# Performance work log

Measured on AMD Instinct MI355X. Metric: run time of the kernel, lower is better.

## Reference

```python
import jax, jax.numpy as jnp
import numpy as np

HEADS = 8
WS = 16
EPS = 1e-6


def setup_inputs() -> dict:
    key = jax.random.key(0)
    k1, k2 = jax.random.split(key)
    x = jax.random.normal(k1, (4, 64, 512, 512), dtype=jnp.float32)
    w_qkv = jax.random.normal(k2, (192, 64), dtype=jnp.float32) * 0.05  # 1x1 conv: [3*dim, dim]
    return {"x": x, "w_qkv": w_qkv}


def _elu1(t):
    return jax.nn.elu(t) + 1.0


def _lwmsa(x, w_qkv):
    B, C, H, W = x.shape
    ws, h = WS, HEADS
    d = C // h
    ph, pw = (-H) % ws, (-W) % ws
    if ph or pw:
        x = jnp.pad(x, ((0, 0), (0, 0), (0, ph), (0, pw)))
    Hp, Wp = H + ph, W + pw
    hh, ww = Hp // ws, Wp // ws
    # 1x1 conv == channel matmul
    qkv = jnp.einsum('oc,bchw->bohw', w_qkv, x)  # [B, 3C, Hp, Wp]
    # 'b (qkv h d) (hh ws1) (ww ws2) -> qkv (b hh ww) h d (ws1 ws2)'
    qkv = qkv.reshape(B, 3, h, d, hh, ws, ww, ws)
    qkv = qkv.transpose(1, 0, 4, 6, 2, 3, 5, 7).reshape(3, B * hh * ww, h, d, ws * ws)
    q, k, v = qkv[0], qkv[1], qkv[2]  # each [Bw, h, d, n]

    feat = None  # carried across heads, [Bw, d, n]
    feats = []
    for i in range(h):
        qi, ki, vi = q[:, i], k[:, i], v[:, i]
        if i > 0:
            qi, ki, vi = qi + feat, ki + feat, vi + feat
        qf = _elu1(qi).transpose(0, 2, 1)   # [Bw, n, d]
        kf = _elu1(ki)                      # [Bw, d, n]
        ksum = jnp.sum(kf, axis=-1) + EPS   # [Bw, d]
        # original: einsum('bhnm,bhc->bhn', q, ksum) sums m and c INDEPENDENTLY
        z = 1.0 / (jnp.sum(qf, axis=-1) * jnp.sum(ksum, axis=-1, keepdims=True))  # [Bw, n]
        kv = jnp.einsum('bdn,bcn->bdc', kf, vi)          # [Bw, d, d]
        feat = jnp.einsum('bnd,bdc,bn->bcn', qf, kv, z)  # [Bw, d, n]
        feats.append(feat)

    out = jnp.stack(feats, axis=1)  # [Bw, h, d, n]
    # '(b hh ww) h d (ws1 ws2) -> b (h d) (hh ws1) (ww ws2)'
    out = out.reshape(B, hh, ww, h, d, ws, ws)
    out = out.transpose(0, 3, 4, 1, 5, 2, 6).reshape(B, C, Hp, Wp)
    return out[:, :, :H, :W]


def reference(x, w_qkv):
    return _lwmsa(x, w_qkv)
```

## Files before the change

### kernel.cpp

```cpp
#include <hip/hip_runtime.h>

#define HW (512 * 512)
#define QP 260
#define WN 12288

typedef __bf16 bf16;
typedef __attribute__((ext_vector_type(8))) __bf16 bf16x8;
typedef __attribute__((ext_vector_type(4))) float f32x4;

__device__ __forceinline__ void cvt_split(float f, bf16& h, bf16& l) {
    h = (bf16)f;
    l = (bf16)(f - (float)h);
}

__global__ __launch_bounds__(256) void wcvt_kernel(
    const float* __restrict__ w, bf16* __restrict__ wh, bf16* __restrict__ wl)
{
    const int i = blockIdx.x * 256 + threadIdx.x;
    if (i < WN) {
        bf16 h, l;
        cvt_split(w[i], h, l);
        wh[i] = h;
        wl[i] = l;
    }
}

__global__ __launch_bounds__(256, 2) void lwmsa_kernel(
    const float* __restrict__ x,
    const bf16* __restrict__ wh,
    const bf16* __restrict__ wl,
    float* __restrict__ out)
{
    const int blk  = blockIdx.x;
    const int b    = blk >> 9;
    const int wrow = (blk >> 4) & 31;
    const int wp   = blk & 15;
    const int n    = threadIdx.x;
    const int lane = n & 63;
    const int wvid = n >> 6;
    const int c16  = lane & 15;
    const int q4   = lane >> 4;

    __shared__ float qk[2][24 * QP];
    __shared__ float kvp[2][4 * 64];
    __shared__ float kv_s[2][64];
    __shared__ float tp[2][2][4];

    int base[2], xwin[2];
    #pragma unroll
    for (int w = 0; w < 2; ++w) {
        const int wcol = wp * 2 + w;
        base[w] = b * (64 * HW) + (wrow * 16 + (n >> 4)) * 512 + wcol * 16 + (n & 15);
        xwin[w] = b * (64 * HW) + (wrow * 16) * 512 + wcol * 16;
    }

    bf16x8 ah[2][2][4], al[2][2][4];
    #pragma unroll
    for (int w = 0; w < 2; ++w)
        #pragma unroll
        for (int ks = 0; ks < 2; ++ks)
            #pragma unroll
            for (int mt = 0; mt < 4; ++mt) {
                const int row = wvid * 4 + mt;
                const float* xp = x + xwin[w] + row * 512 + c16 + (ks * 32 + q4 * 8) * HW;
                #pragma unroll
                for (int j = 0; j < 8; ++j) {
                    bf16 h, l;
                    cvt_split(xp[j * HW], h, l);
                    ah[w][ks][mt][j] = h;
                    al[w][ks][mt][j] = l;
                }
            }

    auto mfma_stage = [&](const bf16x8 (&Ah)[2][4], const bf16x8 (&Al)[2][4],
                          float* __restrict__ qkb, int hh) {
        f32x4 acc[4][2];
        #pragma unroll
        for (int mt = 0; mt < 4; ++mt)
            #pragma unroll
            for (int nt = 0; nt < 2; ++nt)
                acc[mt][nt] = (f32x4){0.f, 0.f, 0.f, 0.f};

        #pragma unroll
        for (int ks = 0; ks < 2; ++ks) {
            #pragma unroll
            for (int nt = 0; nt < 2; ++nt) {
                const int ml   = nt * 16 + c16;
                const int grow = (ml < 24) ? ((ml >> 3) * 64 + hh * 8 + (ml & 7))
                                           : (hh * 8);
                const int off  = grow * 64 + ks * 32 + q4 * 8;
                const bf16x8 bh = *(const bf16x8*)&wh[off];
                const bf16x8 bl = *(const bf16x8*)&wl[off];
                #pragma unroll
                for (int mt = 0; mt < 4; ++mt) {
                    acc[mt][nt] = __builtin_amdgcn_mfma_f32_16x16x32_bf16(Ah[ks][mt], bh, acc[mt][nt], 0, 0, 0);
                    acc[mt][nt] = __builtin_amdgcn_mfma_f32_16x16x32_bf16(Al[ks][mt], bh, acc[mt][nt], 0, 0, 0);
                    acc[mt][nt] = __builtin_amdgcn_mfma_f32_16x16x32_bf16(Ah[ks][mt], bl, acc[mt][nt], 0, 0, 0);
                }
            }
        }

        #pragma unroll
        for (int nt = 0; nt < 2; ++nt) {
            const int ml = nt * 16 + c16;
            if (ml < 24) {
                #pragma unroll
                for (int mt = 0; mt < 4; ++mt) {
                    const int px = (wvid * 4 + mt) * 16 + q4 * 4;
                    *(float4*)&qkb[ml * QP + px] = *(float4*)&acc[mt][nt];
                }
            }
        }
    };

    float feat[2][8];
    #pragma unroll
    for (int w = 0; w < 2; ++w)
        #pragma unroll
        for (int d = 0; d < 8; ++d) feat[w][d] = 0.f;

    mfma_stage(ah[0], al[0], qk[0], 0);
    mfma_stage(ah[1], al[1], qk[1], 0);
    __syncthreads();

    for (int h = 0; h < 8; ++h) {
        float qf[2][8], Sq[2], tpart[2];
        #pragma unroll
        for (int w = 0; w < 2; ++w) {
            Sq[w] = 0.f; tpart[w] = 0.f;
            #pragma unroll
            for (int d = 0; d < 8; ++d) {
                const float aq = qk[w][d * QP + n]        + feat[w][d];
                const float ak = qk[w][(8 + d) * QP + n]  + feat[w][d];
                const float av = qk[w][(16 + d) * QP + n] + feat[w][d];
                qf[w][d] = aq > 0.f ? aq + 1.f : __expf(aq);
                const float kf = ak > 0.f ? ak + 1.f : __expf(ak);
                Sq[w]    += qf[w][d];
                tpart[w] += kf;
                qk[w][(8 + d) * QP + n]  = kf;
                qk[w][(16 + d) * QP + n] = av;
            }
        }

        #pragma unroll
        for (int off = 1; off < 64; off <<= 1) {
            tpart[0] += __shfl_xor(tpart[0], off, 64);
            tpart[1] += __shfl_xor(tpart[1], off, 64);
        }
        if (lane == 0) {
            tp[0][h & 1][wvid] = tpart[0];
            tp[1][h & 1][wvid] = tpart[1];
        }

        asm volatile("s_waitcnt lgkmcnt(0)" ::: "memory");

        #pragma unroll
        for (int w = 0; w < 2; ++w) {
            const float4* kr = (const float4*)(qk[w] + (8 + (lane >> 3)) * QP + wvid * 64);
            const float4* vr = (const float4*)(qk[w] + (16 + (lane & 7)) * QP + wvid * 64);
            float s0 = 0.f, s1 = 0.f, s2 = 0.f, s3 = 0.f;
            #pragma unroll
            for (int j = 0; j < 16; ++j) {
                const float4 kk = kr[j];
                const float4 vv = vr[j];
                s0 = fmaf(kk.x, vv.x, s0);
                s1 = fmaf(kk.y, vv.y, s1);
                s2 = fmaf(kk.z, vv.z, s2);
                s3 = fmaf(kk.w, vv.w, s3);
            }
            kvp[w][wvid * 64 + lane] = (s0 + s1) + (s2 + s3);
        }

        __syncthreads();

        if (n < 64) {
            kv_s[0][n] = (kvp[0][n] + kvp[0][64 + n]) + (kvp[0][128 + n] + kvp[0][192 + n]);
        } else if (n < 128) {
            const int m = n - 64;
            kv_s[1][m] = (kvp[1][m] + kvp[1][64 + m]) + (kvp[1][128 + m] + kvp[1][192 + m]);
        }

        if (h < 7) {
            mfma_stage(ah[0], al[0], qk[0], h + 1);
            mfma_stage(ah[1], al[1], qk[1], h + 1);
        }

        __syncthreads();

        #pragma unroll
        for (int w = 0; w < 2; ++w) {
            const float T  = ((tp[w][h & 1][0] + tp[w][h & 1][1]) +
                              (tp[w][h & 1][2] + tp[w][h & 1][3])) + 8.0f * 1e-6f;
            const float zi = 1.0f / (Sq[w] * T);

            float ft[8];
            #pragma unroll
            for (int d = 0; d < 8; ++d) ft[d] = 0.f;
            #pragma unroll
            for (int d = 0; d < 8; ++d) {
                const float qd = qf[w][d];
                const float4 a  = ((const float4*)(kv_s[w] + d * 8))[0];
                const float4 bb = ((const float4*)(kv_s[w] + d * 8))[1];
                ft[0] = fmaf(qd, a.x,  ft[0]);
                ft[1] = fmaf(qd, a.y,  ft[1]);
                ft[2] = fmaf(qd, a.z,  ft[2]);
                ft[3] = fmaf(qd, a.w,  ft[3]);
                ft[4] = fmaf(qd, bb.x, ft[4]);
                ft[5] = fmaf(qd, bb.y, ft[5]);
                ft[6] = fmaf(qd, bb.z, ft[6]);
                ft[7] = fmaf(qd, bb.w, ft[7]);
            }
            #pragma unroll
            for (int d = 0; d < 8; ++d) {
                feat[w][d] = ft[d] * zi;
                out[base[w] + (h * 8 + d) * HW] = feat[w][d];
            }
        }
    }
}

extern "C" void kernel_launch(void* const* d_in, const int* in_sizes, int n_in,
                              void* d_out, int out_size, void* d_ws, size_t ws_size,
                              hipStream_t stream) {
    const float* x  = (const float*)d_in[0];
    const float* w  = (const float*)d_in[1];
    float* out      = (float*)d_out;
    bf16* wh = (bf16*)d_ws;
    bf16* wl = wh + WN;
    wcvt_kernel<<<dim3((WN + 255) / 256), dim3(256), 0, stream>>>(w, wh, wl);
    lwmsa_kernel<<<dim3(2048), dim3(256), 0, stream>>>(x, wh, wl, out);
}
```

Measured before the change: 256.6 us.

## Stage per-head QKV weight slices in swizzled LDS with double-buffered prefetch

The weight-conversion kernel now writes the hi/lo bf16 weights in a per-head packed order. The main kernel copies each head's slice into LDS through an XOR swizzle, prefetching the next head's slice into registers during the current head's work and writing it to the alternate LDS buffer. MFMA B operands then come from LDS instead of scattered global loads. This adds 12KB of LDS per block, which may affect occupancy at two blocks per CU, plus extra register pressure from the prefetched data.

```diff
diff --git a/kernel.cpp b/kernel.cpp
--- a/kernel.cpp
+++ b/kernel.cpp
@@ -2,7 +2,7 @@
 
 #define HW (512 * 512)
 #define QP 260
-#define WN 12288
+#define WCH 384
 
 typedef __bf16 bf16;
 typedef __attribute__((ext_vector_type(8))) __bf16 bf16x8;
@@ -14,21 +14,26 @@
 }
 
 __global__ __launch_bounds__(256) void wcvt_kernel(
-    const float* __restrict__ w, bf16* __restrict__ wh, bf16* __restrict__ wl)
+    const float* __restrict__ w, bf16* __restrict__ wf)
 {
-    const int i = blockIdx.x * 256 + threadIdx.x;
-    if (i < WN) {
-        bf16 h, l;
-        cvt_split(w[i], h, l);
-        wh[i] = h;
-        wl[i] = l;
-    }
+    const int o = blockIdx.x * 256 + threadIdx.x;
+    if (o >= 8 * WCH * 8) return;
+    const int j  = o & 7;
+    const int s  = (o >> 3) & 7;
+    const int rc = o >> 6;
+    const int r  = rc % 24;
+    const int hp = rc / 24;
+    const int pl = hp & 1;
+    const int h  = hp >> 1;
+    const int grow = (r >> 3) * 64 + h * 8 + (r & 7);
+    bf16 hi, lo;
+    cvt_split(w[grow * 64 + s * 8 + j], hi, lo);
+    wf[o] = pl ? lo : hi;
 }
 
 __global__ __launch_bounds__(256, 2) void lwmsa_kernel(
     const float* __restrict__ x,
-    const bf16* __restrict__ wh,
-    const bf16* __restrict__ wl,
+    const bf16* __restrict__ wf,
     float* __restrict__ out)
 {
     const int blk  = blockIdx.x;
@@ -45,6 +50,7 @@
     __shared__ float kvp[2][4 * 64];
     __shared__ float kv_s[2][64];
     __shared__ float tp[2][2][4];
+    __shared__ bf16  wlds[2 * 3072];
 
     int base[2], xwin[2];
     #pragma unroll
@@ -53,6 +59,16 @@
         base[w] = b * (64 * HW) + (wrow * 16 + (n >> 4)) * 512 + wcol * 16 + (n & 15);
         xwin[w] = b * (64 * HW) + (wrow * 16) * 512 + wcol * 16;
     }
+
+    auto chunk_dst = [](int c) {
+        const int pl = c / 192;
+        const int cc = c % 192;
+        const int r  = cc >> 3;
+        const int s  = cc & 7;
+        return pl * 1536 + (r * 8 + (s ^ (r & 7))) * 8;
+    };
+    const int dst0 = chunk_dst(n);
+    const int dst1 = (n < 128) ? chunk_dst(n + 256) : 0;
 
     bf16x8 ah[2][2][4], al[2][2][4];
     #pragma unroll
@@ -73,7 +89,7 @@
             }
 
     auto mfma_stage = [&](const bf16x8 (&Ah)[2][4], const bf16x8 (&Al)[2][4],
-                          float* __restrict__ qkb, int hh) {
+                          float* __restrict__ qkb, int par) {
         f32x4 acc[4][2];
         #pragma unroll
         for (int mt = 0; mt < 4; ++mt)
@@ -81,16 +97,16 @@
             for (int nt = 0; nt < 2; ++nt)
                 acc[mt][nt] = (f32x4){0.f, 0.f, 0.f, 0.f};
 
+        const bf16* wb = &wlds[par * 3072];
         #pragma unroll
         for (int ks = 0; ks < 2; ++ks) {
             #pragma unroll
             for (int nt = 0; nt < 2; ++nt) {
                 const int ml   = nt * 16 + c16;
-                const int grow = (ml < 24) ? ((ml >> 3) * 64 + hh * 8 + (ml & 7))
-                                           : (hh * 8);
-                const int off  = grow * 64 + ks * 32 + q4 * 8;
-                const bf16x8 bh = *(const bf16x8*)&wh[off];
-                const bf16x8 bl = *(const bf16x8*)&wl[off];
+                const int ml8  = (ml < 24) ? ml : 0;
+                const int slot = (ks * 4 + q4) ^ (ml8 & 7);
+                const bf16x8 bh = *(const bf16x8*)&wb[(ml8 * 8 + slot) * 8];
+                const bf16x8 bl = *(const bf16x8*)&wb[1536 + (ml8 * 8 + slot) * 8];
                 #pragma unroll
                 for (int mt = 0; mt < 4; ++mt) {
                     acc[mt][nt] = __builtin_amdgcn_mfma_f32_16x16x32_bf16(Ah[ks][mt], bh, acc[mt][nt], 0, 0, 0);
@@ -119,11 +135,28 @@
         #pragma unroll
         for (int d = 0; d < 8; ++d) feat[w][d] = 0.f;
 
+    {
+        const float4* wsrc = (const float4*)wf;
+        const float4 c0 = wsrc[n];
+        *(float4*)&wlds[dst0] = c0;
+        if (n < 128) {
+            const float4 c1 = wsrc[n + 256];
+            *(float4*)&wlds[dst1] = c1;
+        }
+    }
+    __syncthreads();
     mfma_stage(ah[0], al[0], qk[0], 0);
     mfma_stage(ah[1], al[1], qk[1], 0);
     __syncthreads();
 
     for (int h = 0; h < 8; ++h) {
+        float4 pc0, pc1;
+        if (h < 7) {
+            const float4* wsrc = (const float4*)(wf + (h + 1) * (WCH * 8));
+            pc0 = wsrc[n];
+            if (n < 128) pc1 = wsrc[n + 256];
+        }
+
         float qf[2][8], Sq[2], tpart[2];
         #pragma unroll
         for (int w = 0; w < 2; ++w) {
@@ -171,6 +204,12 @@
             kvp[w][wvid * 64 + lane] = (s0 + s1) + (s2 + s3);
         }
 
+        if (h < 7) {
+            const int par = (h + 1) & 1;
+            *(float4*)&wlds[par * 3072 + dst0] = pc0;
+            if (n < 128) *(float4*)&wlds[par * 3072 + dst1] = pc1;
+        }
+
         __syncthreads();
 
         if (n < 64) {
@@ -181,8 +220,9 @@
         }
 
         if (h < 7) {
-            mfma_stage(ah[0], al[0], qk[0], h + 1);
-            mfma_stage(ah[1], al[1], qk[1], h + 1);
+            const int par = (h + 1) & 1;
+            mfma_stage(ah[0], al[0], qk[0], par);
+            mfma_stage(ah[1], al[1], qk[1], par);
         }
 
         __syncthreads();
@@ -225,8 +265,7 @@
     const float* x  = (const float*)d_in[0];
     const float* w  = (const float*)d_in[1];
     float* out      = (float*)d_out;
-    bf16* wh = (bf16*)d_ws;
-    bf16* wl = wh + WN;
-    wcvt_kernel<<<dim3((WN + 255) / 256), dim3(256), 0, stream>>>(w, wh, wl);
-    lwmsa_kernel<<<dim3(2048), dim3(256), 0, stream>>>(x, wh, wl, out);
-}
+    bf16* wf = (bf16*)d_ws;
+    wcvt_kernel<<<dim3(96), dim3(256), 0, stream>>>(w, wf);
+    lwmsa_kernel<<<dim3(2048), dim3(256), 0, stream>>>(x, wf, out);
+}
```

Measured after the change: 273.9 us. 1.07x slower.

## Software-pipeline the two windows so each window's MFMA overlaps the other's attention phase

Applied to the files above, without the earlier changes.

The per-head loop is restructured so the two windows handled by a block run staggered. Each half-iteration does the kv finalize and output for one window, the elementwise and kv-partial phase for the other, and the next head's MFMA projection, with weight fragments loaded once per head and shared by both windows. The kv reduction is now done redundantly by every wave into its own shared slot, which removes the serial n<128 step. The aim is to hide MFMA and shared-memory latency behind the other window's work and drop idle time between barriers. The risk is higher register pressure from keeping qf and weight fragments for both windows live, which could spill or lower occupancy at two blocks per SM, plus fragile ordering on the shared tp and kvp buffers.

```diff
diff --git a/kernel.cpp b/kernel.cpp
--- a/kernel.cpp
+++ b/kernel.cpp
@@ -42,9 +42,9 @@
     const int q4   = lane >> 4;
 
     __shared__ float qk[2][24 * QP];
-    __shared__ float kvp[2][4 * 64];
-    __shared__ float kv_s[2][64];
-    __shared__ float tp[2][2][4];
+    __shared__ float kvp[2][256];
+    __shared__ float kv_s[256];
+    __shared__ float tp[2][4];
 
     int base[2], xwin[2];
     #pragma unroll
@@ -72,33 +72,39 @@
                 }
             }
 
-    auto mfma_stage = [&](const bf16x8 (&Ah)[2][4], const bf16x8 (&Al)[2][4],
-                          float* __restrict__ qkb, int hh) {
-        f32x4 acc[4][2];
-        #pragma unroll
-        for (int mt = 0; mt < 4; ++mt)
-            #pragma unroll
-            for (int nt = 0; nt < 2; ++nt)
-                acc[mt][nt] = (f32x4){0.f, 0.f, 0.f, 0.f};
-
-        #pragma unroll
-        for (int ks = 0; ks < 2; ++ks) {
+    bf16x8 bhf[2][2], blf[2][2];
+    auto loadW = [&](int hh) {
+        #pragma unroll
+        for (int ks = 0; ks < 2; ++ks)
             #pragma unroll
             for (int nt = 0; nt < 2; ++nt) {
                 const int ml   = nt * 16 + c16;
                 const int grow = (ml < 24) ? ((ml >> 3) * 64 + hh * 8 + (ml & 7))
                                            : (hh * 8);
                 const int off  = grow * 64 + ks * 32 + q4 * 8;
-                const bf16x8 bh = *(const bf16x8*)&wh[off];
-                const bf16x8 bl = *(const bf16x8*)&wl[off];
+                bhf[ks][nt] = *(const bf16x8*)&wh[off];
+                blf[ks][nt] = *(const bf16x8*)&wl[off];
+            }
+    };
+
+    auto stage = [&](int w) {
+        f32x4 acc[4][2];
+        #pragma unroll
+        for (int mt = 0; mt < 4; ++mt)
+            #pragma unroll
+            for (int nt = 0; nt < 2; ++nt)
+                acc[mt][nt] = (f32x4){0.f, 0.f, 0.f, 0.f};
+
+        #pragma unroll
+        for (int ks = 0; ks < 2; ++ks)
+            #pragma unroll
+            for (int nt = 0; nt < 2; ++nt)
                 #pragma unroll
                 for (int mt = 0; mt < 4; ++mt) {
-                    acc[mt][nt] = __builtin_amdgcn_mfma_f32_16x16x32_bf16(Ah[ks][mt], bh, acc[mt][nt], 0, 0, 0);
-                    acc[mt][nt] = __builtin_amdgcn_mfma_f32_16x16x32_bf16(Al[ks][mt], bh, acc[mt][nt], 0, 0, 0);
-                    acc[mt][nt] = __builtin_amdgcn_mfma_f32_16x16x32_bf16(Ah[ks][mt], bl, acc[mt][nt], 0, 0, 0);
+                    acc[mt][nt] = __builtin_amdgcn_mfma_f32_16x16x32_bf16(ah[w][ks][mt], bhf[ks][nt], acc[mt][nt], 0, 0, 0);
+                    acc[mt][nt] = __builtin_amdgcn_mfma_f32_16x16x32_bf16(al[w][ks][mt], bhf[ks][nt], acc[mt][nt], 0, 0, 0);
+                    acc[mt][nt] = __builtin_amdgcn_mfma_f32_16x16x32_bf16(ah[w][ks][mt], blf[ks][nt], acc[mt][nt], 0, 0, 0);
                 }
-            }
-        }
 
         #pragma unroll
         for (int nt = 0; nt < 2; ++nt) {
@@ -107,7 +113,7 @@
                 #pragma unroll
                 for (int mt = 0; mt < 4; ++mt) {
                     const int px = (wvid * 4 + mt) * 16 + q4 * 4;
-                    *(float4*)&qkb[ml * QP + px] = *(float4*)&acc[mt][nt];
+                    *(float4*)&qk[w][ml * QP + px] = *(float4*)&acc[mt][nt];
                 }
             }
         }
@@ -119,104 +125,99 @@
         #pragma unroll
         for (int d = 0; d < 8; ++d) feat[w][d] = 0.f;
 
-    mfma_stage(ah[0], al[0], qk[0], 0);
-    mfma_stage(ah[1], al[1], qk[1], 0);
+    auto phaseAB = [&](int w, float (&qf)[8], float& Sq) {
+        float tpart = 0.f;
+        Sq = 0.f;
+        #pragma unroll
+        for (int d = 0; d < 8; ++d) {
+            const float aq = qk[w][d * QP + n]        + feat[w][d];
+            const float ak = qk[w][(8 + d) * QP + n]  + feat[w][d];
+            const float av = qk[w][(16 + d) * QP + n] + feat[w][d];
+            qf[d] = aq > 0.f ? aq + 1.f : __expf(aq);
+            const float kf = ak > 0.f ? ak + 1.f : __expf(ak);
+            Sq    += qf[d];
+            tpart += kf;
+            qk[w][(8 + d) * QP + n]  = kf;
+            qk[w][(16 + d) * QP + n] = av;
+        }
+
+        #pragma unroll
+        for (int off = 1; off < 64; off <<= 1)
+            tpart += __shfl_xor(tpart, off, 64);
+        if (lane == 0) tp[w][wvid] = tpart;
+
+        asm volatile("s_waitcnt lgkmcnt(0)" ::: "memory");
+
+        const float4* kr = (const float4*)(qk[w] + (8 + (lane >> 3)) * QP + wvid * 64);
+        const float4* vr = (const float4*)(qk[w] + (16 + (lane & 7)) * QP + wvid * 64);
+        float s0 = 0.f, s1 = 0.f, s2 = 0.f, s3 = 0.f;
+        #pragma unroll
+        for (int j = 0; j < 16; ++j) {
+            const float4 kk = kr[j];
+            const float4 vv = vr[j];
+            s0 = fmaf(kk.x, vv.x, s0);
+            s1 = fmaf(kk.y, vv.y, s1);
+            s2 = fmaf(kk.z, vv.z, s2);
+            s3 = fmaf(kk.w, vv.w, s3);
+        }
+        kvp[w][wvid * 64 + lane] = (s0 + s1) + (s2 + s3);
+    };
+
+    auto phaseD = [&](int w, const float (&qf)[8], float Sq, int h) {
+        const float kvsum = (kvp[w][lane] + kvp[w][64 + lane]) +
+                            (kvp[w][128 + lane] + kvp[w][192 + lane]);
+        kv_s[wvid * 64 + lane] = kvsum;
+        asm volatile("s_waitcnt lgkmcnt(0)" ::: "memory");
+
+        const float T  = ((tp[w][0] + tp[w][1]) + (tp[w][2] + tp[w][3])) + 8.0f * 1e-6f;
+        const float zi = 1.0f / (Sq * T);
+
+        float ft[8];
+        #pragma unroll
+        for (int d = 0; d < 8; ++d) ft[d] = 0.f;
+        #pragma unroll
+        for (int d = 0; d < 8; ++d) {
+            const float qd = qf[d];
+            const float4 a  = ((const float4*)(kv_s + wvid * 64 + d * 8))[0];
+            const float4 bb = ((const float4*)(kv_s + wvid * 64 + d * 8))[1];
+            ft[0] = fmaf(qd, a.x,  ft[0]);
+            ft[1] = fmaf(qd, a.y,  ft[1]);
+            ft[2] = fmaf(qd, a.z,  ft[2]);
+            ft[3] = fmaf(qd, a.w,  ft[3]);
+            ft[4] = fmaf(qd, bb.x, ft[4]);
+            ft[5] = fmaf(qd, bb.y, ft[5]);
+            ft[6] = fmaf(qd, bb.z, ft[6]);
+            ft[7] = fmaf(qd, bb.w, ft[7]);
+        }
+        #pragma unroll
+        for (int d = 0; d < 8; ++d) {
+            feat[w][d] = ft[d] * zi;
+            out[base[w] + (h * 8 + d) * HW] = feat[w][d];
+        }
+    };
+
+    float qf0[8], qf1[8];
+    float Sq0 = 0.f, Sq1 = 0.f;
+
+    loadW(0);
+    stage(0);
     __syncthreads();
 
     for (int h = 0; h < 8; ++h) {
-        float qf[2][8], Sq[2], tpart[2];
-        #pragma unroll
-        for (int w = 0; w < 2; ++w) {
-            Sq[w] = 0.f; tpart[w] = 0.f;
-            #pragma unroll
-            for (int d = 0; d < 8; ++d) {
-                const float aq = qk[w][d * QP + n]        + feat[w][d];
-                const float ak = qk[w][(8 + d) * QP + n]  + feat[w][d];
-                const float av = qk[w][(16 + d) * QP + n] + feat[w][d];
-                qf[w][d] = aq > 0.f ? aq + 1.f : __expf(aq);
-                const float kf = ak > 0.f ? ak + 1.f : __expf(ak);
-                Sq[w]    += qf[w][d];
-                tpart[w] += kf;
-                qk[w][(8 + d) * QP + n]  = kf;
-                qk[w][(16 + d) * QP + n] = av;
-            }
-        }
-
-        #pragma unroll
-        for (int off = 1; off < 64; off <<= 1) {
-            tpart[0] += __shfl_xor(tpart[0], off, 64);
-            tpart[1] += __shfl_xor(tpart[1], off, 64);
-        }
-        if (lane == 0) {
-            tp[0][h & 1][wvid] = tpart[0];
-            tp[1][h & 1][wvid] = tpart[1];
-        }
-
-        asm volatile("s_waitcnt lgkmcnt(0)" ::: "memory");
-
-        #pragma unroll
-        for (int w = 0; w < 2; ++w) {
-            const float4* kr = (const float4*)(qk[w] + (8 + (lane >> 3)) * QP + wvid * 64);
-            const float4* vr = (const float4*)(qk[w] + (16 + (lane & 7)) * QP + wvid * 64);
-            float s0 = 0.f, s1 = 0.f, s2 = 0.f, s3 = 0.f;
-            #pragma unroll
-            for (int j = 0; j < 16; ++j) {
-                const float4 kk = kr[j];
-                const float4 vv = vr[j];
-                s0 = fmaf(kk.x, vv.x, s0);
-                s1 = fmaf(kk.y, vv.y, s1);
-                s2 = fmaf(kk.z, vv.z, s2);
-                s3 = fmaf(kk.w, vv.w, s3);
-            }
-            kvp[w][wvid * 64 + lane] = (s0 + s1) + (s2 + s3);
-        }
-
+        loadW(h);
+        if (h > 0) phaseD(1, qf1, Sq1, h - 1);
+        phaseAB(0, qf0, Sq0);
+        stage(1);
         __syncthreads();
 
-        if (n < 64) {
-            kv_s[0][n] = (kvp[0][n] + kvp[0][64 + n]) + (kvp[0][128 + n] + kvp[0][192 + n]);
-        } else if (n < 128) {
-            const int m = n - 64;
-            kv_s[1][m] = (kvp[1][m] + kvp[1][64 + m]) + (kvp[1][128 + m] + kvp[1][192 + m]);
-        }
-
-        if (h < 7) {
-            mfma_stage(ah[0], al[0], qk[0], h + 1);
-            mfma_stage(ah[1], al[1], qk[1], h + 1);
-        }
-
+        if (h < 7) loadW(h + 1);
+        phaseD(0, qf0, Sq0, h);
+        phaseAB(1, qf1, Sq1);
+        if (h < 7) stage(0);
         __syncthreads();
-
-        #pragma unroll
-        for (int w = 0; w < 2; ++w) {
-            const float T  = ((tp[w][h & 1][0] + tp[w][h & 1][1]) +
-                              (tp[w][h & 1][2] + tp[w][h & 1][3])) + 8.0f * 1e-6f;
-            const float zi = 1.0f / (Sq[w] * T);
-
-            float ft[8];
-            #pragma unroll
-            for (int d = 0; d < 8; ++d) ft[d] = 0.f;
-            #pragma unroll
-            for (int d = 0; d < 8; ++d) {
-                const float qd = qf[w][d];
-                const float4 a  = ((const float4*)(kv_s[w] + d * 8))[0];
-                const float4 bb = ((const float4*)(kv_s[w] + d * 8))[1];
-                ft[0] = fmaf(qd, a.x,  ft[0]);
-                ft[1] = fmaf(qd, a.y,  ft[1]);
-                ft[2] = fmaf(qd, a.z,  ft[2]);
-                ft[3] = fmaf(qd, a.w,  ft[3]);
-                ft[4] = fmaf(qd, bb.x, ft[4]);
-                ft[5] = fmaf(qd, bb.y, ft[5]);
-                ft[6] = fmaf(qd, bb.z, ft[6]);
-                ft[7] = fmaf(qd, bb.w, ft[7]);
-            }
-            #pragma unroll
-            for (int d = 0; d < 8; ++d) {
-                feat[w][d] = ft[d] * zi;
-                out[base[w] + (h * 8 + d) * HW] = feat[w][d];
-            }
-        }
     }
+
+    phaseD(1, qf1, Sq1, 7);
 }
 
 extern "C" void kernel_launch(void* const* d_in, const int* in_sizes, int n_in,
```

After: 297.0 us. 15.8% more time.
